# Kernel tuning notes

Hardware: AMD Instinct MI355X
Metric: run time of the kernel (lower is better)

The kernel has to match this reference:

```python
import jax, jax.numpy as jnp
import numpy as np

NUM_HEADS = 4
NUM_GROUPS = 32
EPS = 1e-5


def setup_inputs() -> dict:
    key = jax.random.key(0)
    k1, k2, k3 = jax.random.split(key, 3)
    C = 256
    x = jax.random.normal(k1, (2, C, 64, 64), dtype=jnp.float32)
    gn_scale = jnp.ones((C,), dtype=jnp.float32)
    gn_bias = jnp.zeros((C,), dtype=jnp.float32)
    # 1x1 convs are plain channel-mixing matmuls; init like torch kaiming-uniform-ish
    w_qkv = jax.random.normal(k2, (3 * C, C), dtype=jnp.float32) * (1.0 / np.sqrt(C))
    w_proj = jax.random.normal(k3, (C, C), dtype=jnp.float32) * (1.0 / np.sqrt(C))
    b_proj = jnp.zeros((C,), dtype=jnp.float32)
    return {"x": x, "gn_scale": gn_scale, "gn_bias": gn_bias,
            "w_qkv": w_qkv, "w_proj": w_proj, "b_proj": b_proj}


def _group_norm(x, scale, bias):
    b, c, h, w = x.shape
    xg = x.reshape(b, NUM_GROUPS, c // NUM_GROUPS, h, w)
    mean = xg.mean(axis=(2, 3, 4), keepdims=True)
    var = xg.var(axis=(2, 3, 4), keepdims=True)
    xn = ((xg - mean) * jax.lax.rsqrt(var + EPS)).reshape(b, c, h, w)
    return xn * scale[:, None, None] + bias[:, None, None]


def reference(x, gn_scale, gn_bias, w_qkv, w_proj, b_proj):
    b, c, h, w = x.shape
    hd = c // NUM_HEADS
    scale = hd ** -0.5
    n = h * w

    hn = _group_norm(x, gn_scale, gn_bias)
    # 1x1 conv == channel matmul: (3c, c) @ (b, c, h*w)
    qkv = jnp.einsum('oc,bcn->bon', w_qkv, hn.reshape(b, c, n))
    qkv = qkv.reshape(b, 3, NUM_HEADS, hd, n)
    q, k, v = qkv[:, 0], qkv[:, 1], qkv[:, 2]  # each (b, H, hd, n)

    # scores: (b, H, n, n); softmax over keys (last axis)
    scores = jnp.einsum('bhdn,bhdm->bhnm', q, k) * scale
    attn = jax.nn.softmax(scores, axis=-1)
    out = jnp.einsum('bhnm,bhdm->bhdn', attn, v)  # (b, H, hd, n)
    out = out.reshape(b, c, h, w)

    proj = jnp.einsum('oc,bcn->bon', w_proj, out.reshape(b, c, n)).reshape(b, c, h, w)
    return proj + b_proj[:, None, None] + x
```

## Files before the change

kernel.cpp:

```cpp
#include <hip/hip_runtime.h>
#include <hip/hip_bf16.h>
#include <math.h>

#define Bdim 2
#define Cdim 256
#define Ndim 4096
#define HEADS 4
#define HDim 64

typedef _Float16 half8 __attribute__((ext_vector_type(8)));
typedef _Float16 half4 __attribute__((ext_vector_type(4)));
typedef float f32x4 __attribute__((ext_vector_type(4)));

static const size_t WS_STATS  = 0;
static const size_t WS_WTPROJ = 256;
static const size_t WS_WHQ    = 65792;
static const size_t WS_HN     = 164096;
static const size_t WS_HNT    = 2261248;
static const size_t WS_QT     = 3309824;
static const size_t WS_KT     = 4358400;
static const size_t WS_VF     = 5406976;

#define QSCALE 0.18033688f
#define SINIT  -8.65617025f

__global__ __launch_bounds__(256) void gn_stats_k(const float* __restrict__ x,
                                                  float* __restrict__ stats) {
    int g = blockIdx.x;
    const float4* p4 = (const float4*)(x + (size_t)g * 32768);
    int tid = threadIdx.x;
    float s = 0.f, ss = 0.f;
#pragma unroll 8
    for (int w = 0; w < 32; w++) {
        float4 v = p4[tid + w * 256];
        s += v.x + v.y + v.z + v.w;
        ss += v.x * v.x + v.y * v.y + v.z * v.z + v.w * v.w;
    }
#pragma unroll
    for (int m = 1; m < 64; m <<= 1) {
        s += __shfl_xor(s, m);
        ss += __shfl_xor(ss, m);
    }
    __shared__ float ws_s[4], ws_ss[4];
    int wid = tid >> 6, lane = tid & 63;
    if (lane == 0) { ws_s[wid] = s; ws_ss[wid] = ss; }
    __syncthreads();
    if (tid == 0) {
        float ts = ws_s[0] + ws_s[1] + ws_s[2] + ws_s[3];
        float tss = ws_ss[0] + ws_ss[1] + ws_ss[2] + ws_ss[3];
        float mean = ts * (1.0f / 32768.0f);
        float var = tss * (1.0f / 32768.0f) - mean * mean;
        stats[2 * g] = mean;
        stats[2 * g + 1] = rsqrtf(var + 1e-5f);
    }
}

__global__ __launch_bounds__(256) void gnT_k(const float* __restrict__ x,
                                             const float* __restrict__ stats,
                                             const float* __restrict__ scale,
                                             const float* __restrict__ bias,
                                             _Float16* __restrict__ hnT) {
    __shared__ float t[64][68];
    const int tid = threadIdx.x;
    const int n0 = blockIdx.x << 6, c0 = blockIdx.y << 6, bz = blockIdx.z;
    const int cr = tid >> 2, q4 = tid & 3;
    const int c = c0 + cr;
    const int g = bz * 32 + (c >> 3);
    const float sc = stats[2 * g + 1] * scale[c];
    const float bi = bias[c] - stats[2 * g] * sc;
    const float* base = x + ((size_t)(bz * 256 + c)) * Ndim + n0;
#pragma unroll
    for (int k = 0; k < 4; k++) {
        int j = k * 4 + q4;
        float4 v = *(const float4*)(base + j * 4);
        v.x = v.x * sc + bi; v.y = v.y * sc + bi; v.z = v.z * sc + bi; v.w = v.w * sc + bi;
        *(float4*)&t[cr][j * 4] = v;
    }
    __syncthreads();
    const int nr = tid >> 2, ch = tid & 3;
    half8 o0, o1;
#pragma unroll
    for (int j = 0; j < 8; j++) o0[j] = (_Float16)t[ch * 16 + j][nr];
#pragma unroll
    for (int j = 0; j < 8; j++) o1[j] = (_Float16)t[ch * 16 + 8 + j][nr];
    _Float16* dst = hnT + ((size_t)bz * Ndim + n0 + nr) * 256 + c0 + ch * 16;
    *(half8*)(dst) = o0;
    *(half8*)(dst + 8) = o1;
}

__global__ __launch_bounds__(256) void wcvt_k(const float* __restrict__ w,
                                              _Float16* __restrict__ wh) {
    int i = blockIdx.x * 256 + threadIdx.x;
    float v = w[i];
    if ((i >> 8) < 256) v *= QSCALE;
    wh[i] = (_Float16)v;
}

__global__ __launch_bounds__(256) void tpose_k(const float* __restrict__ W,
                                               float* __restrict__ WT,
                                               int O, int Cc) {
    __shared__ float t[32][33];
    int c0 = blockIdx.x * 32, o0 = blockIdx.y * 32;
    int tx = threadIdx.x, ty = threadIdx.y;
#pragma unroll
    for (int k = 0; k < 4; k++) {
        int o = o0 + ty + k * 8;
        t[ty + k * 8][tx] = W[(size_t)o * Cc + c0 + tx];
    }
    __syncthreads();
#pragma unroll
    for (int k = 0; k < 4; k++) {
        int c = c0 + ty + k * 8;
        WT[(size_t)c * O + o0 + tx] = t[tx][ty + k * 8];
    }
}

__global__ __launch_bounds__(256) void gemm_qkv16_k(const _Float16* __restrict__ wh,
                                                    const _Float16* __restrict__ hnT,
                                                    _Float16* __restrict__ qT,
                                                    _Float16* __restrict__ kT,
                                                    _Float16* __restrict__ vF) {
    __shared__ __align__(16) char smem[32768];
    const int tid = threadIdx.x, w = tid >> 6, lane = tid & 63;
    const int a = lane >> 4, b_ = lane & 15;
    const int wo = w >> 1, wn = w & 1;
    const int n0 = blockIdx.x << 7, o0 = blockIdx.y << 7, bz = blockIdx.z;

    const int srow = tid >> 1, su = (tid & 1) << 1;
    const _Float16* wg = wh + (size_t)(o0 + srow) * 256 + (su << 3);
    const _Float16* xg = hnT + ((size_t)(bz * Ndim + n0 + srow)) * 256 + (su << 3);
    const int wd0 = srow * 64 + ((su ^ (srow & 3)) << 4);
    const int wd1 = srow * 64 + (((su + 1) ^ (srow & 3)) << 4);

    {
        half8 a0 = *(const half8*)(wg), a1 = *(const half8*)(wg + 8);
        half8 b0 = *(const half8*)(xg), b1 = *(const half8*)(xg + 8);
        *(half8*)(smem + wd0) = a0; *(half8*)(smem + wd1) = a1;
        *(half8*)(smem + 16384 + wd0) = b0; *(half8*)(smem + 16384 + wd1) = b1;
    }
    __syncthreads();

    f32x4 acc[4][4] = {};
    const int fa = (a ^ (b_ & 3)) << 4;
    int arow[4], brow[4];
#pragma unroll
    for (int t = 0; t < 4; t++) {
        arow[t] = (wo * 64 + t * 16 + b_) * 64 + fa;
        brow[t] = 16384 + (wn * 64 + t * 16 + b_) * 64 + fa;
    }

    for (int kk = 0; kk < 8; kk++) {
        const int cur = (kk & 1) * 8192;
        half8 nw0, nw1, nx0, nx1;
        const bool pf = (kk < 7);
        if (pf) {
            const _Float16* wp = wg + (kk + 1) * 32;
            const _Float16* xp = xg + (kk + 1) * 32;
            nw0 = *(const half8*)(wp); nw1 = *(const half8*)(wp + 8);
            nx0 = *(const half8*)(xp); nx1 = *(const half8*)(xp + 8);
        }
        half8 af[4], bf[4];
#pragma unroll
        for (int t = 0; t < 4; t++) {
            af[t] = *(const half8*)(smem + cur + arow[t]);
            bf[t] = *(const half8*)(smem + cur + brow[t]);
        }
#pragma unroll
        for (int i = 0; i < 4; i++)
#pragma unroll
            for (int j = 0; j < 4; j++)
                acc[i][j] = __builtin_amdgcn_mfma_f32_16x16x32_f16(af[i], bf[j], acc[i][j], 0, 0, 0);
        if (pf) {
            const int nxt = cur ^ 8192;
            *(half8*)(smem + nxt + wd0) = nw0; *(half8*)(smem + nxt + wd1) = nw1;
            *(half8*)(smem + 16384 + nxt + wd0) = nx0; *(half8*)(smem + 16384 + nxt + wd1) = nx1;
        }
        __syncthreads();
    }

    if (o0 < 512) {
#pragma unroll
        for (int ot = 0; ot < 4; ot++) {
#pragma unroll
            for (int nt = 0; nt < 4; nt++) {
                int n = wn * 64 + nt * 16 + b_;
                int u = wo * 16 + ot * 4 + a;
                half4 hv;
                hv[0] = (_Float16)acc[ot][nt][0]; hv[1] = (_Float16)acc[ot][nt][1];
                hv[2] = (_Float16)acc[ot][nt][2]; hv[3] = (_Float16)acc[ot][nt][3];
                *(half4*)(smem + n * 256 + ((u ^ (n & 31)) << 3)) = hv;
            }
        }
        __syncthreads();
        _Float16* dst = (o0 >= 256) ? kT : qT;
        const int headbase = (o0 >> 6) & 3;
#pragma unroll
        for (int hsel = 0; hsel < 2; hsel++) {
            _Float16* hb = dst + ((size_t)(bz * 4 + headbase + hsel)) * (Ndim * 64);
#pragma unroll
            for (int p = 0; p < 4; p++) {
                int n = p * 32 + (tid >> 3), j = tid & 7;
                int u0 = hsel * 16 + j * 2;
                half4 lo = *(const half4*)(smem + n * 256 + ((u0 ^ (n & 31)) << 3));
                half4 hi = *(const half4*)(smem + n * 256 + (((u0 + 1) ^ (n & 31)) << 3));
                half8 o8;
                o8[0] = lo[0]; o8[1] = lo[1]; o8[2] = lo[2]; o8[3] = lo[3];
                o8[4] = hi[0]; o8[5] = hi[1]; o8[6] = hi[2]; o8[7] = hi[3];
                *(half8*)(hb + (size_t)(n0 + n) * 64 + j * 8) = o8;
            }
        }
    } else {
        _Float16* vb = vF + ((size_t)bz * 256 + (o0 - 512)) * Ndim;
#pragma unroll
        for (int ot = 0; ot < 4; ot++)
#pragma unroll
            for (int nt = 0; nt < 4; nt++)
#pragma unroll
                for (int r = 0; r < 4; r++)
                    vb[(size_t)(wo * 64 + ot * 16 + a * 4 + r) * Ndim +
                       n0 + wn * 64 + nt * 16 + b_] = (_Float16)acc[ot][nt][r];
    }
}

__global__ __launch_bounds__(256) void attn_k(const _Float16* __restrict__ qT,
                                              const _Float16* __restrict__ kT,
                                              const _Float16* __restrict__ vF,
                                              float* __restrict__ outp) {
    __shared__ __align__(16) char smem[16384];
    const int tid = threadIdx.x;
    const int w = tid >> 6, lane = tid & 63;
    const int a = lane >> 4, b_ = lane & 15;
    const int s = blockIdx.x;
    const int o = ((s & 7) << 6) + (s >> 3);
    const int qt = o & 63;
    const size_t bh = (size_t)(o >> 6);
    const int q0 = qt << 6;
    const _Float16* Qb = qT + bh * (size_t)(Ndim * 64);
    const _Float16* Kb = kT + bh * (size_t)(Ndim * 64);
    const _Float16* Vb = vF + bh * (size_t)(64 * Ndim);

    const _Float16* qp = Qb + (size_t)(q0 + w * 16 + b_) * 64 + a * 8;
    half8 qf0 = *(const half8*)(qp);
    half8 qf1 = *(const half8*)(qp + 32);

    const int km = tid >> 3, kj = tid & 7;
    const int kldso = ((km << 3) | (kj ^ (km & 7))) << 4;
    const char* kgp = (const char*)Kb + (size_t)km * 128 + kj * 16;
    const int vd = tid >> 2, vj = tid & 3;
    const int vldso = 8192 + (((vd << 2) | (vj ^ ((vd >> 1) & 3))) << 4);
    const char* vgp = (const char*)Vb + (size_t)vd * (Ndim * 2) + vj * 16;

    const int swk = b_ & 7;
    const int k00o = ((b_ << 3) | (a ^ swk)) << 4;
    const int k01o = ((b_ << 3) | ((a + 4) ^ swk)) << 4;
    const int k10o = (((16 + b_) << 3) | (a ^ swk)) << 4;
    const int k11o = (((16 + b_) << 3) | ((a + 4) ^ swk)) << 4;
    const int xsw = (b_ >> 1) & 3;
    int vlo[4], vhi[4];
#pragma unroll
    for (int dt = 0; dt < 4; dt++) {
        int d = 16 * dt + b_;
        vlo[dt] = 8192 + d * 64 + ((((a >> 1)) ^ xsw) << 4) + ((a & 1) << 3);
        vhi[dt] = 8192 + d * 64 + (((2 + (a >> 1)) ^ xsw) << 4) + ((a & 1) << 3);
    }

    f32x4 oa[4] = {};
    float lr = 0.f;

    {
        f32x4 k0v = *(const f32x4*)kgp;
        f32x4 v0v = *(const f32x4*)vgp;
        kgp += 4096; vgp += 64;
        *(f32x4*)(smem + kldso) = k0v;
        *(f32x4*)(smem + vldso) = v0v;
    }
    __syncthreads();

    for (int it = 0; it < 128; ++it) {
        const int cur = (it & 1) << 12;
        f32x4 kn, vn;
        const bool pf = (it < 127);
        if (pf) {
            kn = *(const f32x4*)kgp; kgp += 4096;
            vn = *(const f32x4*)vgp; vgp += 64;
        }
        const char* Kc = smem + cur;
        half8 k00 = *(const half8*)(Kc + k00o);
        half8 k01 = *(const half8*)(Kc + k01o);
        half8 k10 = *(const half8*)(Kc + k10o);
        half8 k11 = *(const half8*)(Kc + k11o);

        f32x4 s0 = {SINIT, SINIT, SINIT, SINIT}, s1 = s0;
        s0 = __builtin_amdgcn_mfma_f32_16x16x32_f16(k00, qf0, s0, 0, 0, 0);
        s0 = __builtin_amdgcn_mfma_f32_16x16x32_f16(k01, qf1, s0, 0, 0, 0);
        s1 = __builtin_amdgcn_mfma_f32_16x16x32_f16(k10, qf0, s1, 0, 0, 0);
        s1 = __builtin_amdgcn_mfma_f32_16x16x32_f16(k11, qf1, s1, 0, 0, 0);

        float e0[4], e1[4];
#pragma unroll
        for (int r = 0; r < 4; r++) {
            e0[r] = __builtin_exp2f(s0[r]);
            e1[r] = __builtin_exp2f(s1[r]);
        }
        lr += ((e0[0] + e0[1]) + (e0[2] + e0[3])) + ((e1[0] + e1[1]) + (e1[2] + e1[3]));

        half4 alo, ahi;
#pragma unroll
        for (int r = 0; r < 4; r++) { alo[r] = (_Float16)e0[r]; ahi[r] = (_Float16)e1[r]; }

        const char* Vc = smem + cur;
#pragma unroll
        for (int dt = 0; dt < 4; dt++) {
            half4 bl = *(const half4*)(Vc + vlo[dt]);
            half4 bh2 = *(const half4*)(Vc + vhi[dt]);
            oa[dt] = __builtin_amdgcn_mfma_f32_16x16x16f16(alo, bl, oa[dt], 0, 0, 0);
            oa[dt] = __builtin_amdgcn_mfma_f32_16x16x16f16(ahi, bh2, oa[dt], 0, 0, 0);
        }

        if (pf) {
            const int nxt = cur ^ 4096;
            *(f32x4*)(smem + nxt + kldso) = kn;
            *(f32x4*)(smem + nxt + vldso) = vn;
        }
        __syncthreads();
    }

    float lrt = lr;
    lrt += __shfl_xor(lrt, 16);
    lrt += __shfl_xor(lrt, 32);
    float inv[4];
#pragma unroll
    for (int r = 0; r < 4; r++) inv[r] = 1.0f / __shfl(lrt, a * 4 + r);

    char* LoB = smem;
#pragma unroll
    for (int dt = 0; dt < 4; dt++) {
        f32x4 val = oa[dt];
#pragma unroll
        for (int r = 0; r < 4; r++) val[r] *= inv[r];
        int d = 16 * dt + b_;
        int off = (d * 256 + w * 64 + a * 16) ^ ((d & 7) << 4);
        *(f32x4*)(LoB + off) = val;
    }
    __syncthreads();
#pragma unroll
    for (int p = 0; p < 4; p++) {
        int d = p * 16 + (tid >> 4), qc = tid & 15;
        int off = (d * 256 + qc * 16) ^ ((d & 7) << 4);
        f32x4 v = *(const f32x4*)(LoB + off);
        *(f32x4*)(outp + (bh * 64 + d) * (size_t)Ndim + q0 + (qc << 2)) = v;
    }
}

__global__ __launch_bounds__(256) void gemm_proj_k(const float* __restrict__ WT,
                                                   const float* __restrict__ X,
                                                   float* __restrict__ out,
                                                   const float* __restrict__ bias,
                                                   const float* __restrict__ resid) {
    __shared__ __align__(16) float Ws[32][128];
    __shared__ __align__(16) float Xs[32][128];
    const int tid = threadIdx.x, tx = tid & 15, ty = tid >> 4;
    const int n0 = blockIdx.x << 7, o0 = blockIdx.y << 7;
    const size_t bX = (size_t)blockIdx.z * Cdim * Ndim;
    float acc[8][8] = {};
    for (int k0 = 0; k0 < Cdim; k0 += 32) {
        __syncthreads();
#pragma unroll
        for (int kq = 0; kq < 4; kq++) {
            int f4 = tid + (kq << 8);
            int r = f4 >> 5, cc = (f4 & 31) << 2;
            *(float4*)&Ws[r][cc] = *(const float4*)(WT + (size_t)(k0 + r) * 256 + o0 + cc);
            *(float4*)&Xs[r][cc] = *(const float4*)(X + bX + (size_t)(k0 + r) * Ndim + n0 + cc);
        }
        __syncthreads();
#pragma unroll 4
        for (int kk = 0; kk < 32; kk++) {
            float4 wa = *(const float4*)&Ws[kk][ty << 2];
            float4 wb = *(const float4*)&Ws[kk][(ty << 2) + 64];
            float4 xa = *(const float4*)&Xs[kk][tx << 2];
            float4 xb = *(const float4*)&Xs[kk][(tx << 2) + 64];
            float wv[8] = {wa.x, wa.y, wa.z, wa.w, wb.x, wb.y, wb.z, wb.w};
            float xv[8] = {xa.x, xa.y, xa.z, xa.w, xb.x, xb.y, xb.z, xb.w};
#pragma unroll
            for (int i = 0; i < 8; i++)
#pragma unroll
                for (int j = 0; j < 8; j++)
                    acc[i][j] = fmaf(wv[i], xv[j], acc[i][j]);
        }
    }
#pragma unroll
    for (int i = 0; i < 8; i++) {
        int o = o0 + (ty << 2) + ((i < 4) ? i : (64 + i - 4));
        size_t rowoff = bX + (size_t)o * Ndim + n0 + (tx << 2);
        float bv = bias[o];
        float4 r0, r1;
        r0.x = acc[i][0] + bv; r0.y = acc[i][1] + bv; r0.z = acc[i][2] + bv; r0.w = acc[i][3] + bv;
        r1.x = acc[i][4] + bv; r1.y = acc[i][5] + bv; r1.z = acc[i][6] + bv; r1.w = acc[i][7] + bv;
        float4 x0 = *(const float4*)(resid + rowoff);
        float4 x1 = *(const float4*)(resid + rowoff + 64);
        r0.x += x0.x; r0.y += x0.y; r0.z += x0.z; r0.w += x0.w;
        r1.x += x1.x; r1.y += x1.y; r1.z += x1.z; r1.w += x1.w;
        *(float4*)(out + rowoff) = r0;
        *(float4*)(out + rowoff + 64) = r1;
    }
}

extern "C" void kernel_launch(void* const* d_in, const int* in_sizes, int n_in,
                              void* d_out, int out_size, void* d_ws, size_t ws_size,
                              hipStream_t stream) {
    (void)in_sizes; (void)n_in; (void)out_size; (void)ws_size;
    const float* x        = (const float*)d_in[0];
    const float* gn_scale = (const float*)d_in[1];
    const float* gn_bias  = (const float*)d_in[2];
    const float* w_qkv    = (const float*)d_in[3];
    const float* w_proj   = (const float*)d_in[4];
    const float* b_proj   = (const float*)d_in[5];
    float* ws    = (float*)d_ws;
    float* stats = ws + WS_STATS;
    float* wtp   = ws + WS_WTPROJ;
    _Float16* whq = (_Float16*)(ws + WS_WHQ);
    float* hn    = ws + WS_HN;
    _Float16* hnT = (_Float16*)(ws + WS_HNT);
    _Float16* qT = (_Float16*)(ws + WS_QT);
    _Float16* kT = (_Float16*)(ws + WS_KT);
    _Float16* vF = (_Float16*)(ws + WS_VF);
    float* outp  = (float*)d_out;

    gn_stats_k<<<64, 256, 0, stream>>>(x, stats);
    gnT_k<<<dim3(64, 4, 2), 256, 0, stream>>>(x, stats, gn_scale, gn_bias, hnT);
    wcvt_k<<<768, 256, 0, stream>>>(w_qkv, whq);
    tpose_k<<<dim3(8, 8), dim3(32, 8), 0, stream>>>(w_proj, wtp, 256, 256);
    gemm_qkv16_k<<<dim3(32, 6, 2), 256, 0, stream>>>(whq, hnT, qT, kT, vF);
    attn_k<<<512, 256, 0, stream>>>(qT, kT, vF, hn);
    gemm_proj_k<<<dim3(32, 2, 2), 256, 0, stream>>>(wtp, hn, outp, b_proj, x);
}
```

Before: 214.1 us.

## Split attention keys across warps with register-direct K/V loads and LDS reduction

The attention kernel now gives each of the four warps a quarter of the key range for all 64 queries, instead of giving each warp 16 queries over all keys. K and V fragments are loaded straight from global memory into registers with a two-stage software pipeline, which removes the per-iteration LDS staging and block-wide barriers. Partial outputs and row sums from the warps are combined through LDS at the end before normalisation. The cost is much higher register pressure (16 accumulator tiles per warp, launch bounds set to 2) and uncoalesced, non-shared global fragment loads, since each warp reads its own keys.

```diff
diff --git a/kernel.cpp b/kernel.cpp
--- a/kernel.cpp
+++ b/kernel.cpp
@@ -222,11 +222,52 @@
     }
 }
 
-__global__ __launch_bounds__(256) void attn_k(const _Float16* __restrict__ qT,
-                                              const _Float16* __restrict__ kT,
-                                              const _Float16* __restrict__ vF,
-                                              float* __restrict__ outp) {
-    __shared__ __align__(16) char smem[16384];
+#define LOADKV(S, st)                                                        \
+    {                                                                        \
+        const _Float16* kp_ = Kp + (size_t)(st) * 2048;                      \
+        S##k00 = *(const half8*)(kp_);                                       \
+        S##k01 = *(const half8*)(kp_ + 32);                                  \
+        S##k10 = *(const half8*)(kp_ + 1024);                                \
+        S##k11 = *(const half8*)(kp_ + 1024 + 32);                           \
+        const _Float16* vp_ = Vp + (st) * 32;                                \
+        _Pragma("unroll") for (int dt = 0; dt < 4; dt++) {                   \
+            S##v[dt][0] = *(const half4*)(vp_ + dt * 16 * Ndim);             \
+            S##v[dt][1] = *(const half4*)(vp_ + dt * 16 * Ndim + 16);        \
+        }                                                                    \
+    }
+
+#define COMPUTE(S)                                                                        \
+    {                                                                                     \
+        _Pragma("unroll") for (int qi = 0; qi < 4; qi++) {                                \
+            f32x4 s0 = {SINIT, SINIT, SINIT, SINIT}, s1 = s0;                             \
+            s0 = __builtin_amdgcn_mfma_f32_16x16x32_f16(S##k00, qf0[qi], s0, 0, 0, 0);    \
+            s0 = __builtin_amdgcn_mfma_f32_16x16x32_f16(S##k01, qf1[qi], s0, 0, 0, 0);    \
+            s1 = __builtin_amdgcn_mfma_f32_16x16x32_f16(S##k10, qf0[qi], s1, 0, 0, 0);    \
+            s1 = __builtin_amdgcn_mfma_f32_16x16x32_f16(S##k11, qf1[qi], s1, 0, 0, 0);    \
+            half4 alo, ahi;                                                               \
+            float rs = 0.f;                                                               \
+            _Pragma("unroll") for (int r = 0; r < 4; r++) {                               \
+                float e0 = __builtin_exp2f(s0[r]);                                        \
+                float e1 = __builtin_exp2f(s1[r]);                                        \
+                rs += e0 + e1;                                                            \
+                alo[r] = (_Float16)e0;                                                    \
+                ahi[r] = (_Float16)e1;                                                    \
+            }                                                                             \
+            lr[qi] += rs;                                                                 \
+            _Pragma("unroll") for (int dt = 0; dt < 4; dt++) {                            \
+                oa[qi][dt] = __builtin_amdgcn_mfma_f32_16x16x16f16(alo, S##v[dt][0],      \
+                                                                   oa[qi][dt], 0, 0, 0); \
+                oa[qi][dt] = __builtin_amdgcn_mfma_f32_16x16x16f16(ahi, S##v[dt][1],      \
+                                                                   oa[qi][dt], 0, 0, 0); \
+            }                                                                             \
+        }                                                                                 \
+    }
+
+__global__ __launch_bounds__(256, 2) void attn_k(const _Float16* __restrict__ qT,
+                                                 const _Float16* __restrict__ kT,
+                                                 const _Float16* __restrict__ vF,
+                                                 float* __restrict__ outp) {
+    __shared__ __align__(16) char smem[33792];
     const int tid = threadIdx.x;
     const int w = tid >> 6, lane = tid & 63;
     const int a = lane >> 4, b_ = lane & 15;
@@ -239,116 +280,91 @@
     const _Float16* Kb = kT + bh * (size_t)(Ndim * 64);
     const _Float16* Vb = vF + bh * (size_t)(64 * Ndim);
 
-    const _Float16* qp = Qb + (size_t)(q0 + w * 16 + b_) * 64 + a * 8;
-    half8 qf0 = *(const half8*)(qp);
-    half8 qf1 = *(const half8*)(qp + 32);
-
-    const int km = tid >> 3, kj = tid & 7;
-    const int kldso = ((km << 3) | (kj ^ (km & 7))) << 4;
-    const char* kgp = (const char*)Kb + (size_t)km * 128 + kj * 16;
-    const int vd = tid >> 2, vj = tid & 3;
-    const int vldso = 8192 + (((vd << 2) | (vj ^ ((vd >> 1) & 3))) << 4);
-    const char* vgp = (const char*)Vb + (size_t)vd * (Ndim * 2) + vj * 16;
-
-    const int swk = b_ & 7;
-    const int k00o = ((b_ << 3) | (a ^ swk)) << 4;
-    const int k01o = ((b_ << 3) | ((a + 4) ^ swk)) << 4;
-    const int k10o = (((16 + b_) << 3) | (a ^ swk)) << 4;
-    const int k11o = (((16 + b_) << 3) | ((a + 4) ^ swk)) << 4;
-    const int xsw = (b_ >> 1) & 3;
-    int vlo[4], vhi[4];
-#pragma unroll
-    for (int dt = 0; dt < 4; dt++) {
-        int d = 16 * dt + b_;
-        vlo[dt] = 8192 + d * 64 + ((((a >> 1)) ^ xsw) << 4) + ((a & 1) << 3);
-        vhi[dt] = 8192 + d * 64 + (((2 + (a >> 1)) ^ xsw) << 4) + ((a & 1) << 3);
-    }
-
-    f32x4 oa[4] = {};
-    float lr = 0.f;
+    half8 qf0[4], qf1[4];
+#pragma unroll
+    for (int qi = 0; qi < 4; qi++) {
+        const _Float16* qp = Qb + (size_t)(q0 + qi * 16 + b_) * 64 + a * 8;
+        qf0[qi] = *(const half8*)(qp);
+        qf1[qi] = *(const half8*)(qp + 32);
+    }
+
+    const int kb = w << 10;
+    const _Float16* Kp = Kb + (size_t)(kb + b_) * 64 + a * 8;
+    const _Float16* Vp = Vb + (size_t)b_ * Ndim + kb + a * 4;
+
+    f32x4 oa[4][4] = {};
+    float lr[4] = {0.f, 0.f, 0.f, 0.f};
+
+    half8 Ak00, Ak01, Ak10, Ak11; half4 Av[4][2];
+    half8 Bk00, Bk01, Bk10, Bk11; half4 Bv[4][2];
+
+    LOADKV(A, 0);
+    for (int st = 0; st < 32; st += 2) {
+        LOADKV(B, st + 1);
+        COMPUTE(A);
+        if (st + 2 < 32) LOADKV(A, st + 2);
+        COMPUTE(B);
+    }
+
+    float lrw[4];
+#pragma unroll
+    for (int qi = 0; qi < 4; qi++) {
+        float t = lr[qi];
+        t += __shfl_xor(t, 16);
+        t += __shfl_xor(t, 32);
+        lrw[qi] = t;
+    }
+    float* lrs = (float*)(smem + 32768);
+    if (a == 0) {
+#pragma unroll
+        for (int qi = 0; qi < 4; qi++) lrs[w * 64 + qi * 16 + b_] = lrw[qi];
+    }
+
+    float* Ow = (float*)(smem + ((w & 1) << 14));
+    if (w < 2) {
+#pragma unroll
+        for (int qi = 0; qi < 4; qi++)
+#pragma unroll
+            for (int dt = 0; dt < 4; dt++) {
+                int off = (16 * dt + b_) * 64 + (((qi * 4 + a) ^ b_) << 2);
+                *(f32x4*)(Ow + off) = oa[qi][dt];
+            }
+    }
+    __syncthreads();
+    if (w >= 2) {
+#pragma unroll
+        for (int qi = 0; qi < 4; qi++)
+#pragma unroll
+            for (int dt = 0; dt < 4; dt++) {
+                int off = (16 * dt + b_) * 64 + (((qi * 4 + a) ^ b_) << 2);
+                f32x4 v = *(const f32x4*)(Ow + off);
+                v += oa[qi][dt];
+                *(f32x4*)(Ow + off) = v;
+            }
+    }
+    __syncthreads();
 
     {
-        f32x4 k0v = *(const f32x4*)kgp;
-        f32x4 v0v = *(const f32x4*)vgp;
-        kgp += 4096; vgp += 64;
-        *(f32x4*)(smem + kldso) = k0v;
-        *(f32x4*)(smem + vldso) = v0v;
-    }
-    __syncthreads();
-
-    for (int it = 0; it < 128; ++it) {
-        const int cur = (it & 1) << 12;
-        f32x4 kn, vn;
-        const bool pf = (it < 127);
-        if (pf) {
-            kn = *(const f32x4*)kgp; kgp += 4096;
-            vn = *(const f32x4*)vgp; vgp += 64;
-        }
-        const char* Kc = smem + cur;
-        half8 k00 = *(const half8*)(Kc + k00o);
-        half8 k01 = *(const half8*)(Kc + k01o);
-        half8 k10 = *(const half8*)(Kc + k10o);
-        half8 k11 = *(const half8*)(Kc + k11o);
-
-        f32x4 s0 = {SINIT, SINIT, SINIT, SINIT}, s1 = s0;
-        s0 = __builtin_amdgcn_mfma_f32_16x16x32_f16(k00, qf0, s0, 0, 0, 0);
-        s0 = __builtin_amdgcn_mfma_f32_16x16x32_f16(k01, qf1, s0, 0, 0, 0);
-        s1 = __builtin_amdgcn_mfma_f32_16x16x32_f16(k10, qf0, s1, 0, 0, 0);
-        s1 = __builtin_amdgcn_mfma_f32_16x16x32_f16(k11, qf1, s1, 0, 0, 0);
-
-        float e0[4], e1[4];
-#pragma unroll
-        for (int r = 0; r < 4; r++) {
-            e0[r] = __builtin_exp2f(s0[r]);
-            e1[r] = __builtin_exp2f(s1[r]);
-        }
-        lr += ((e0[0] + e0[1]) + (e0[2] + e0[3])) + ((e1[0] + e1[1]) + (e1[2] + e1[3]));
-
-        half4 alo, ahi;
-#pragma unroll
-        for (int r = 0; r < 4; r++) { alo[r] = (_Float16)e0[r]; ahi[r] = (_Float16)e1[r]; }
-
-        const char* Vc = smem + cur;
-#pragma unroll
-        for (int dt = 0; dt < 4; dt++) {
-            half4 bl = *(const half4*)(Vc + vlo[dt]);
-            half4 bh2 = *(const half4*)(Vc + vhi[dt]);
-            oa[dt] = __builtin_amdgcn_mfma_f32_16x16x16f16(alo, bl, oa[dt], 0, 0, 0);
-            oa[dt] = __builtin_amdgcn_mfma_f32_16x16x16f16(ahi, bh2, oa[dt], 0, 0, 0);
-        }
-
-        if (pf) {
-            const int nxt = cur ^ 4096;
-            *(f32x4*)(smem + nxt + kldso) = kn;
-            *(f32x4*)(smem + nxt + vldso) = vn;
-        }
-        __syncthreads();
-    }
-
-    float lrt = lr;
-    lrt += __shfl_xor(lrt, 16);
-    lrt += __shfl_xor(lrt, 32);
-    float inv[4];
-#pragma unroll
-    for (int r = 0; r < 4; r++) inv[r] = 1.0f / __shfl(lrt, a * 4 + r);
-
-    char* LoB = smem;
-#pragma unroll
-    for (int dt = 0; dt < 4; dt++) {
-        f32x4 val = oa[dt];
-#pragma unroll
-        for (int r = 0; r < 4; r++) val[r] *= inv[r];
-        int d = 16 * dt + b_;
-        int off = (d * 256 + w * 64 + a * 16) ^ ((d & 7) << 4);
-        *(f32x4*)(LoB + off) = val;
-    }
-    __syncthreads();
-#pragma unroll
-    for (int p = 0; p < 4; p++) {
-        int d = p * 16 + (tid >> 4), qc = tid & 15;
-        int off = (d * 256 + qc * 16) ^ ((d & 7) << 4);
-        f32x4 v = *(const f32x4*)(LoB + off);
-        *(f32x4*)(outp + (bh * 64 + d) * (size_t)Ndim + q0 + (qc << 2)) = v;
+        const float* R0 = (const float*)(smem);
+        const float* R1 = (const float*)(smem + 16384);
+        int dr = tid >> 4, qc = tid & 15;
+        f32x4 lt = *(const f32x4*)(lrs + qc * 4);
+        lt += *(const f32x4*)(lrs + 64 + qc * 4);
+        lt += *(const f32x4*)(lrs + 128 + qc * 4);
+        lt += *(const f32x4*)(lrs + 192 + qc * 4);
+        f32x4 inv;
+#pragma unroll
+        for (int r = 0; r < 4; r++) inv[r] = 1.0f / lt[r];
+#pragma unroll
+        for (int p = 0; p < 4; p++) {
+            int d = p * 16 + dr;
+            int off = d * 64 + ((qc ^ (d & 15)) << 2);
+            f32x4 v = *(const f32x4*)(R0 + off);
+            v += *(const f32x4*)(R1 + off);
+#pragma unroll
+            for (int r = 0; r < 4; r++) v[r] *= inv[r];
+            *(f32x4*)(outp + (bh * 64 + d) * (size_t)Ndim + q0 + (qc << 2)) = v;
+        }
     }
 }
 
```

Measured after the change: 231.9 us. +8.3%, slower.
